# Kernel optimization log

Measured on AMD Instinct MI355X. Metric: run time of the kernel, lower is better.

## Reference

```python
import jax, jax.numpy as jnp
import numpy as np

L, B, T, D, H, F, V = 8, 2, 1024, 1024, 16, 4096, 50257


def _ln(x, w, b):
    m = jnp.mean(x, axis=-1, keepdims=True)
    v = jnp.mean((x - m) ** 2, axis=-1, keepdims=True)
    return (x - m) * jax.lax.rsqrt(v + 1e-5) * w + b


def setup_inputs() -> dict:
    key = jax.random.key(0)
    ks = iter(jax.random.split(key, 16))
    s = jnp.float32(0.02)
    w = lambda shape: jax.random.normal(next(ks), shape, jnp.float32) * s
    return {
        'idx': jax.random.randint(next(ks), (B, T), 0, V, jnp.int32),
        'emb': w((V, D)),
        'pos_emb': w((T, D)),
        'ln1_w': jnp.ones((L, D), jnp.float32),
        'ln1_b': jnp.zeros((L, D), jnp.float32),
        'qkv_w': w((L, D, 3 * D)),
        'qkv_b': jnp.zeros((L, 3 * D), jnp.float32),
        'ln2_w': jnp.ones((L, D), jnp.float32),
        'ln2_b': jnp.zeros((L, D), jnp.float32),
        'fc1_w': w((L, D, F)),
        'fc1_b': jnp.zeros((L, F), jnp.float32),
        'fc2_w': w((L, F, D)),
        'fc2_b': jnp.zeros((L, D), jnp.float32),
        'lnf_w': jnp.ones((D,), jnp.float32),
        'lnf_b': jnp.zeros((D,), jnp.float32),
        'head_w': w((D, V)),
        'head_b': jnp.zeros((V,), jnp.float32),
    }


def reference(idx, emb, pos_emb, ln1_w, ln1_b, qkv_w, qkv_b, ln2_w, ln2_b,
              fc1_w, fc1_b, fc2_w, fc2_b, lnf_w, lnf_b, head_w, head_b):
    b, t = idx.shape
    d = emb.shape[1]
    hd = d // H
    x = emb[idx] + pos_emb[:t]                      # [b,t,d]
    mask = jnp.tril(jnp.ones((t, t), bool))         # causal mask
    inv_scale = jnp.float32(1.0 / (d ** 0.5))       # NOTE: source scales by sqrt(full dim), not head_dim

    def layer(x, p):
        l1w, l1b, qw, qb, l2w, l2b, f1w, f1b, f2w, f2b = p
        h = _ln(x, l1w, l1b)
        qkv = h @ qw + qb                           # [b,t,3d]
        q, k, v = jnp.split(qkv, 3, axis=-1)
        q = q.reshape(b, t, H, hd)
        k = k.reshape(b, t, H, hd)
        v = v.reshape(b, t, H, hd)
        logits = jnp.einsum('bqhe,bkhe->bhqk', q, k) * inv_scale
        logits = jnp.where(mask, logits, -jnp.inf)
        attn = jax.nn.softmax(logits, axis=-1)
        o = jnp.einsum('bhqk,bkhe->bqhe', attn, v).reshape(b, t, d)
        x = x + o                                   # no output projection in source
        h = _ln(x, l2w, l2b)
        h = jax.nn.gelu(h @ f1w + f1b, approximate=False)
        h = jax.nn.gelu(h @ f2w + f2b, approximate=False)  # GELU after fc2 too, per source
        return x + h, None

    x, _ = jax.lax.scan(
        layer, x,
        (ln1_w, ln1_b, qkv_w, qkv_b, ln2_w, ln2_b, fc1_w, fc1_b, fc2_w, fc2_b))
    x = _ln(x, lnf_w, lnf_b)
    return x @ head_w + head_b                      # [b,t,V] logits
```

## Files before the change

kernel.cpp:

```cpp
#include <hip/hip_runtime.h>
#include <math.h>

#define Ln 8
#define Bn 2
#define Tn 1024
#define Dm 1024
#define Hn 16
#define Fm 4096
#define Vn 50257
#define NTOK 2048

typedef unsigned short u16;
typedef u16   u16x8  __attribute__((ext_vector_type(8)));
typedef __bf16 bf16x8 __attribute__((ext_vector_type(8)));
typedef float f32x4  __attribute__((ext_vector_type(4)));

__device__ __forceinline__ u16 f2bf(float f){
  unsigned u = __builtin_bit_cast(unsigned, f);
  u += 0x7FFFu + ((u >> 16) & 1u);
  return (u16)(u >> 16);
}
__device__ __forceinline__ float bf2f(u16 s){
  return __builtin_bit_cast(float, ((unsigned)s) << 16);
}
__device__ __forceinline__ float gelu_f(float v){
  return 0.5f * v * (1.0f + erff(v * 0.70710678118654752440f));
}
__device__ __forceinline__ void gload16(const void* g, void* l){
  __builtin_amdgcn_global_load_lds(
      (const __attribute__((address_space(1))) void*)g,
      (__attribute__((address_space(3))) void*)l, 16, 0, 0);
}

__global__ __launch_bounds__(256) void embed_kernel(const int* __restrict__ idx,
                                                    const float* __restrict__ emb,
                                                    const float* __restrict__ pos,
                                                    float* __restrict__ x){
  int row = blockIdx.x;
  int t = row & (Tn - 1);
  int id = idx[row];
  const float4* e = (const float4*)(emb + (size_t)id * Dm);
  const float4* p = (const float4*)(pos + (size_t)t * Dm);
  float4* o = (float4*)(x + (size_t)row * Dm);
  int i = threadIdx.x;
  float4 a = e[i], b = p[i];
  o[i] = make_float4(a.x + b.x, a.y + b.y, a.z + b.z, a.w + b.w);
}

__global__ __launch_bounds__(256) void ln_kernel(const float* __restrict__ xin,
                                                 const float* __restrict__ w,
                                                 const float* __restrict__ bb,
                                                 u16* __restrict__ out){
  int row = blockIdx.x;
  int t = threadIdx.x;
  float4 v = ((const float4*)(xin + (size_t)row * Dm))[t];
  float s  = v.x + v.y + v.z + v.w;
  float s2 = v.x*v.x + v.y*v.y + v.z*v.z + v.w*v.w;
  #pragma unroll
  for (int off = 1; off < 64; off <<= 1){
    s  += __shfl_xor(s, off);
    s2 += __shfl_xor(s2, off);
  }
  __shared__ float red[8];
  int wv = t >> 6, lane = t & 63;
  if (lane == 0){ red[wv] = s; red[4 + wv] = s2; }
  __syncthreads();
  s  = red[0] + red[1] + red[2] + red[3];
  s2 = red[4] + red[5] + red[6] + red[7];
  float mean = s * (1.0f / Dm);
  float var  = s2 * (1.0f / Dm) - mean * mean;
  float rs = rsqrtf(var + 1e-5f);
  float4 wv4 = ((const float4*)w)[t];
  float4 bv4 = ((const float4*)bb)[t];
  u16 o4[4];
  o4[0] = f2bf((v.x - mean) * rs * wv4.x + bv4.x);
  o4[1] = f2bf((v.y - mean) * rs * wv4.y + bv4.y);
  o4[2] = f2bf((v.z - mean) * rs * wv4.z + bv4.z);
  o4[3] = f2bf((v.w - mean) * rs * wv4.w + bv4.w);
  *(uint2*)(out + (size_t)row * Dm + t * 4) = *(uint2*)o4;
}

__global__ __launch_bounds__(256) void transpose_w(const float* __restrict__ Bw,
                                                   u16* __restrict__ Bt,
                                                   int N, int K, int c0){
  int n0 = blockIdx.x * 64, k0 = blockIdx.y * 64;
  __shared__ float tile[64][66];
  int t = threadIdx.x;
  int rr = t >> 4, nc = (t & 15) * 4;
  #pragma unroll
  for (int u = 0; u < 4; u++){
    int kk = rr + u * 16;
    int gn = c0 + n0 + nc;
    const float* src = Bw + (size_t)(k0 + kk) * N;
    float4 v;
    if (gn + 3 < N) v = *(const float4*)(src + gn);
    else {
      v.x = (gn     < N) ? src[gn]     : 0.0f;
      v.y = (gn + 1 < N) ? src[gn + 1] : 0.0f;
      v.z = (gn + 2 < N) ? src[gn + 2] : 0.0f;
      v.w = (gn + 3 < N) ? src[gn + 3] : 0.0f;
    }
    tile[kk][nc]     = v.x;
    tile[kk][nc + 1] = v.y;
    tile[kk][nc + 2] = v.z;
    tile[kk][nc + 3] = v.w;
  }
  __syncthreads();
  int np = t >> 2, c = t & 3;
  u16* dst = Bt + (size_t)(n0 + np) * K + k0;
  u16 pk[8];
  #pragma unroll
  for (int j = 0; j < 8; j++) pk[j] = f2bf(tile[c*8 + j][np]);
  *(int4*)(dst + c*8) = *(int4*)pk;
  #pragma unroll
  for (int j = 0; j < 8; j++) pk[j] = f2bf(tile[32 + c*8 + j][np]);
  *(int4*)(dst + 32 + c*8) = *(int4*)pk;
}

#define BM 128
#define BN 128
template<int MODE>
__global__ __launch_bounds__(256) void gemm_kernel(const u16* __restrict__ A,
                                                   const u16* __restrict__ Bt,
                                                   const float* __restrict__ bias,
                                                   void* __restrict__ outp,
                                                   float* __restrict__ resid,
                                                   u16* __restrict__ vT,
                                                   int K, int Nout, int c0){
  __shared__ u16 sA[128][64];
  __shared__ u16 sB[128][64];
  int t = threadIdx.x;
  int lane = t & 63, w = t >> 6;
  int wm = w >> 1, wn = w & 1;
  int lr = lane & 15, lg = lane >> 4;
  int m0 = blockIdx.y * BM, n0 = blockIdx.x * BN;

  f32x4 acc[4][4] = {};

  int srow = lane >> 3, scol = (lane & 7) * 8;
  int cswz = ((lr >> 2) & 3) << 4;

  for (int k0 = 0; k0 < K; k0 += 64){
    __syncthreads();
    #pragma unroll
    for (int i = 0; i < 4; i++){
      int rbase = i*32 + w*8;
      int r = rbase + srow;
      int gc = scol ^ (((r >> 2) & 3) << 4);
      gload16(A  + (size_t)(m0 + r) * K + k0 + gc, (char*)&sA[rbase][0]);
      gload16(Bt + (size_t)(n0 + r) * K + k0 + gc, (char*)&sB[rbase][0]);
    }
    __syncthreads();
    #pragma unroll
    for (int kk = 0; kk < 2; kk++){
      bf16x8 af[4], bfr[4];
      #pragma unroll
      for (int i = 0; i < 4; i++) af[i]  = *(const bf16x8*)&sA[wm*64 + i*16 + lr][(kk*32 + lg*8) ^ cswz];
      #pragma unroll
      for (int j = 0; j < 4; j++) bfr[j] = *(const bf16x8*)&sB[wn*64 + j*16 + lr][(kk*32 + lg*8) ^ cswz];
      #pragma unroll
      for (int i = 0; i < 4; i++)
        #pragma unroll
        for (int j = 0; j < 4; j++)
          acc[i][j] = __builtin_amdgcn_mfma_f32_16x16x32_bf16(af[i], bfr[j], acc[i][j], 0, 0, 0);
    }
  }

  #pragma unroll
  for (int i = 0; i < 4; i++){
    int gr0 = m0 + wm*64 + i*16 + lg*4;
    #pragma unroll
    for (int j = 0; j < 4; j++){
      int gc = c0 + n0 + wn*64 + j*16 + lr;
      if (MODE == 3 && gc >= Nout) continue;
      float bb = bias[gc];
      if (MODE == 0 && gc >= 2048){
        int hh = (gc - 2048) >> 6, dd = (gc - 2048) & 63;
        int b_ = gr0 >> 10, tt = gr0 & 1023;
        u16 pk[4];
        #pragma unroll
        for (int r = 0; r < 4; r++) pk[r] = f2bf(acc[i][j][r] + bb);
        *(uint2*)&vT[((size_t)((b_*Hn + hh)*64 + dd))*Tn + tt] = *(uint2*)pk;
        continue;
      }
      #pragma unroll
      for (int r = 0; r < 4; r++){
        float v = acc[i][j][r] + bb;
        size_t oi = (size_t)(gr0 + r) * Nout + gc;
        if (MODE == 0)      ((u16*)outp)[oi] = f2bf(v);
        else if (MODE == 1) ((u16*)outp)[oi] = f2bf(gelu_f(v));
        else if (MODE == 2) resid[oi] = resid[oi] + gelu_f(v);
        else                ((float*)outp)[oi] = v;
      }
    }
  }
}

__global__ __launch_bounds__(256) void attn_mfma(const u16* __restrict__ qkv,
                                                 const u16* __restrict__ vT,
                                                 float* __restrict__ x){
  int bh = blockIdx.x;
  int b = bh >> 4, h_ = bh & 15;
  int qt = blockIdx.y;
  int t = threadIdx.x;
  int w = t >> 6, lane = t & 63;
  int lr = lane & 15, lg = lane >> 4;

  __shared__ u16 sK [2][64][72];
  __shared__ u16 sVt[2][64][72];
  __shared__ u16 sP [64][72];

  const u16* qbase = qkv + ((size_t)(b*Tn + qt*64 + w*16 + lr)) * 3*Dm + h_*64 + lg*8;
  bf16x8 qf[2];
  qf[0] = *(const bf16x8*)(qbase);
  qf[1] = *(const bf16x8*)(qbase + 32);

  f32x4 o_[4] = {};
  float m_[4], l_[4];
  #pragma unroll
  for (int r = 0; r < 4; r++){ m_[r] = -INFINITY; l_[r] = 0.0f; }

  int sr = t >> 2, sc = (t & 3) * 16;
  const u16* kbase = qkv + ((size_t)(b*Tn + sr)) * 3*Dm + Dm + h_*64 + sc;
  const u16* vbase = vT + ((size_t)(bh*64 + sr)) * Tn + sc;
  int4 kr0, kr1, vr0, vr1;

  kr0 = *(const int4*)(kbase);     kr1 = *(const int4*)(kbase + 8);
  vr0 = *(const int4*)(vbase);     vr1 = *(const int4*)(vbase + 8);
  *(int4*)&sK [0][sr][sc]     = kr0;  *(int4*)&sK [0][sr][sc + 8] = kr1;
  *(int4*)&sVt[0][sr][sc]     = vr0;  *(int4*)&sVt[0][sr][sc + 8] = vr1;

  const float sc_ = 0.03125f;
  for (int kt = 0; kt <= qt; kt++){
    int cur = kt & 1;
    if (kt < qt){
      const u16* kb = kbase + (size_t)(kt + 1) * 64 * 3 * Dm;
      const u16* vb = vbase + (kt + 1) * 64;
      kr0 = *(const int4*)(kb);    kr1 = *(const int4*)(kb + 8);
      vr0 = *(const int4*)(vb);    vr1 = *(const int4*)(vb + 8);
    }
    __syncthreads();

    f32x4 s[4] = {};
    #pragma unroll
    for (int kf = 0; kf < 2; kf++){
      #pragma unroll
      for (int nf = 0; nf < 4; nf++){
        bf16x8 kfrag = *(const bf16x8*)&sK[cur][nf*16 + lr][kf*32 + lg*8];
        s[nf] = __builtin_amdgcn_mfma_f32_16x16x32_bf16(qf[kf], kfrag, s[nf], 0, 0, 0);
      }
    }

    bool lastt = (kt == qt);
    float tmax[4] = {-INFINITY, -INFINITY, -INFINITY, -INFINITY};
    #pragma unroll
    for (int nf = 0; nf < 4; nf++)
      #pragma unroll
      for (int r = 0; r < 4; r++){
        float v = s[nf][r] * sc_;
        if (lastt){
          int kkg = nf*16 + lr, qg = w*16 + lg*4 + r;
          if (kkg > qg) v = -INFINITY;
        }
        s[nf][r] = v;
        tmax[r] = fmaxf(tmax[r], v);
      }
    #pragma unroll
    for (int r = 0; r < 4; r++){
      tmax[r] = fmaxf(tmax[r], __shfl_xor(tmax[r], 1));
      tmax[r] = fmaxf(tmax[r], __shfl_xor(tmax[r], 2));
      tmax[r] = fmaxf(tmax[r], __shfl_xor(tmax[r], 4));
      tmax[r] = fmaxf(tmax[r], __shfl_xor(tmax[r], 8));
    }
    float resc[4], psum[4];
    #pragma unroll
    for (int r = 0; r < 4; r++){
      float nm = fmaxf(m_[r], tmax[r]);
      resc[r] = __expf(m_[r] - nm);
      m_[r] = nm;
      psum[r] = 0.0f;
    }
    #pragma unroll
    for (int nf = 0; nf < 4; nf++)
      #pragma unroll
      for (int r = 0; r < 4; r++){
        float pv = __expf(s[nf][r] - m_[r]);
        s[nf][r] = pv;
        psum[r] += pv;
      }
    #pragma unroll
    for (int r = 0; r < 4; r++){
      psum[r] += __shfl_xor(psum[r], 1);
      psum[r] += __shfl_xor(psum[r], 2);
      psum[r] += __shfl_xor(psum[r], 4);
      psum[r] += __shfl_xor(psum[r], 8);
      l_[r] = l_[r] * resc[r] + psum[r];
    }
    #pragma unroll
    for (int df = 0; df < 4; df++)
      #pragma unroll
      for (int r = 0; r < 4; r++)
        o_[df][r] *= resc[r];

    #pragma unroll
    for (int nf = 0; nf < 4; nf++)
      #pragma unroll
      for (int r = 0; r < 4; r++)
        sP[w*16 + lg*4 + r][nf*16 + lr] = f2bf(s[nf][r]);

    #pragma unroll
    for (int kf = 0; kf < 2; kf++){
      bf16x8 pfrag = *(const bf16x8*)&sP[w*16 + lr][kf*32 + lg*8];
      #pragma unroll
      for (int df = 0; df < 4; df++){
        bf16x8 vfrag = *(const bf16x8*)&sVt[cur][df*16 + lr][kf*32 + lg*8];
        o_[df] = __builtin_amdgcn_mfma_f32_16x16x32_bf16(pfrag, vfrag, o_[df], 0, 0, 0);
      }
    }

    if (kt < qt){
      int nxt = cur ^ 1;
      *(int4*)&sK [nxt][sr][sc]     = kr0;  *(int4*)&sK [nxt][sr][sc + 8] = kr1;
      *(int4*)&sVt[nxt][sr][sc]     = vr0;  *(int4*)&sVt[nxt][sr][sc + 8] = vr1;
    }
  }

  float inv[4];
  #pragma unroll
  for (int r = 0; r < 4; r++) inv[r] = 1.0f / l_[r];
  #pragma unroll
  for (int df = 0; df < 4; df++)
    #pragma unroll
    for (int r = 0; r < 4; r++){
      float* xr = x + ((size_t)(b*Tn + qt*64 + w*16 + lg*4 + r)) * Dm + h_*64 + df*16 + lr;
      *xr += o_[df][r] * inv[r];
    }
}

extern "C" void kernel_launch(void* const* d_in, const int* in_sizes, int n_in,
                              void* d_out, int out_size, void* d_ws, size_t ws_size,
                              hipStream_t stream){
  const int*   idx   = (const int*)  d_in[0];
  const float* emb   = (const float*)d_in[1];
  const float* pos   = (const float*)d_in[2];
  const float* ln1w  = (const float*)d_in[3];
  const float* ln1b  = (const float*)d_in[4];
  const float* qkvw  = (const float*)d_in[5];
  const float* qkvb  = (const float*)d_in[6];
  const float* ln2w  = (const float*)d_in[7];
  const float* ln2b  = (const float*)d_in[8];
  const float* fc1w  = (const float*)d_in[9];
  const float* fc1b  = (const float*)d_in[10];
  const float* fc2w  = (const float*)d_in[11];
  const float* fc2b  = (const float*)d_in[12];
  const float* lnfw  = (const float*)d_in[13];
  const float* lnfb  = (const float*)d_in[14];
  const float* headw = (const float*)d_in[15];
  const float* headb = (const float*)d_in[16];
  float* out = (float*)d_out;

  char* ws = (char*)d_ws;
  float* x   = (float*)(ws);
  u16*   h   = (u16*)  (ws + (8u  << 20));
  u16*   qkv = (u16*)  (ws + (12u << 20));
  u16*   f1  = (u16*)  (ws + (24u << 20));
  u16*   Bt  = (u16*)  (ws + (40u << 20));
  u16*   vT  = (u16*)  (ws + (48u << 20));

  embed_kernel<<<NTOK, 256, 0, stream>>>(idx, emb, pos, x);

  for (int l = 0; l < Ln; l++){
    ln_kernel<<<NTOK, 256, 0, stream>>>(x, ln1w + l*Dm, ln1b + l*Dm, h);
    transpose_w<<<dim3(3072/64, Dm/64), 256, 0, stream>>>(qkvw + (size_t)l*Dm*3072, Bt, 3072, Dm, 0);
    gemm_kernel<0><<<dim3(3072/BN, NTOK/BM), 256, 0, stream>>>(h, Bt, qkvb + l*3072, qkv, nullptr, vT, Dm, 3072, 0);
    attn_mfma<<<dim3(Bn*Hn, Tn/64), 256, 0, stream>>>(qkv, vT, x);
    ln_kernel<<<NTOK, 256, 0, stream>>>(x, ln2w + l*Dm, ln2b + l*Dm, h);
    transpose_w<<<dim3(Fm/64, Dm/64), 256, 0, stream>>>(fc1w + (size_t)l*Dm*Fm, Bt, Fm, Dm, 0);
    gemm_kernel<1><<<dim3(Fm/BN, NTOK/BM), 256, 0, stream>>>(h, Bt, fc1b + l*Fm, f1, nullptr, nullptr, Dm, Fm, 0);
    transpose_w<<<dim3(Dm/64, Fm/64), 256, 0, stream>>>(fc2w + (size_t)l*Fm*Dm, Bt, Dm, Fm, 0);
    gemm_kernel<2><<<dim3(Dm/BN, NTOK/BM), 256, 0, stream>>>(f1, Bt, fc2b + l*Dm, nullptr, x, nullptr, Fm, Dm, 0);
  }

  ln_kernel<<<NTOK, 256, 0, stream>>>(x, lnfw, lnfb, h);

  const int CHUNK = 4096;
  for (int c0 = 0; c0 < Vn; c0 += CHUNK){
    int W = Vn - c0; if (W > CHUNK) W = CHUNK;
    int ngx = (W + BN - 1) / BN;
    transpose_w<<<dim3(ngx * 2, Dm/64), 256, 0, stream>>>(headw, Bt, Vn, Dm, c0);
    gemm_kernel<3><<<dim3(ngx, NTOK/BM), 256, 0, stream>>>(h, Bt, headb, out, nullptr, nullptr, Dm, Vn, c0);
  }
}
```

Before: 2.144 ms.

## Reorder attention blocks heaviest-first, prescale Q, raise MFMA priority, single head GEMM

The attention grid is flattened to 512 blocks and ordered so the longest causal query tiles are scheduled first, which targets load imbalance at the tail. The softmax scale is folded into Q when it is loaded, s_setprio brackets the MFMA sections, and the LM-head weight transpose and GEMM run as one launch over the full vocabulary when the workspace is large enough, replacing 13 chunked launch pairs. Folding the scale into Q before rounding to bf16 changes rounding slightly, and the single head path depends on the workspace size check.

```diff
diff --git a/kernel.cpp b/kernel.cpp
--- a/kernel.cpp
+++ b/kernel.cpp
@@ -199,9 +199,11 @@
 __global__ __launch_bounds__(256) void attn_mfma(const u16* __restrict__ qkv,
                                                  const u16* __restrict__ vT,
                                                  float* __restrict__ x){
-  int bh = blockIdx.x;
+  int bid = blockIdx.x;
+  int bh = bid & 31;
+  int j = bid >> 5;
+  int qt = (j < 8) ? (15 - j) : (j - 8);
   int b = bh >> 4, h_ = bh & 15;
-  int qt = blockIdx.y;
   int t = threadIdx.x;
   int w = t >> 6, lane = t & 63;
   int lr = lane & 15, lg = lane >> 4;
@@ -212,25 +214,28 @@
 
   const u16* qbase = qkv + ((size_t)(b*Tn + qt*64 + w*16 + lr)) * 3*Dm + h_*64 + lg*8;
   bf16x8 qf[2];
-  qf[0] = *(const bf16x8*)(qbase);
-  qf[1] = *(const bf16x8*)(qbase + 32);
+  #pragma unroll
+  for (int i = 0; i < 2; i++){
+    u16x8 raw = *(const u16x8*)(qbase + i * 32);
+    #pragma unroll
+    for (int u = 0; u < 8; u++) qf[i][u] = (__bf16)(bf2f(raw[u]) * 0.03125f);
+  }
 
   f32x4 o_[4] = {};
   float m_[4], l_[4];
   #pragma unroll
   for (int r = 0; r < 4; r++){ m_[r] = -INFINITY; l_[r] = 0.0f; }
 
-  int sr = t >> 2, sc = (t & 3) * 16;
-  const u16* kbase = qkv + ((size_t)(b*Tn + sr)) * 3*Dm + Dm + h_*64 + sc;
-  const u16* vbase = vT + ((size_t)(bh*64 + sr)) * Tn + sc;
+  int sr = t >> 2, scc = (t & 3) * 16;
+  const u16* kbase = qkv + ((size_t)(b*Tn + sr)) * 3*Dm + Dm + h_*64 + scc;
+  const u16* vbase = vT + ((size_t)(bh*64 + sr)) * Tn + scc;
   int4 kr0, kr1, vr0, vr1;
 
   kr0 = *(const int4*)(kbase);     kr1 = *(const int4*)(kbase + 8);
   vr0 = *(const int4*)(vbase);     vr1 = *(const int4*)(vbase + 8);
-  *(int4*)&sK [0][sr][sc]     = kr0;  *(int4*)&sK [0][sr][sc + 8] = kr1;
-  *(int4*)&sVt[0][sr][sc]     = vr0;  *(int4*)&sVt[0][sr][sc + 8] = vr1;
-
-  const float sc_ = 0.03125f;
+  *(int4*)&sK [0][sr][scc]     = kr0;  *(int4*)&sK [0][sr][scc + 8] = kr1;
+  *(int4*)&sVt[0][sr][scc]     = vr0;  *(int4*)&sVt[0][sr][scc + 8] = vr1;
+
   for (int kt = 0; kt <= qt; kt++){
     int cur = kt & 1;
     if (kt < qt){
@@ -242,6 +247,7 @@
     __syncthreads();
 
     f32x4 s[4] = {};
+    __builtin_amdgcn_s_setprio(1);
     #pragma unroll
     for (int kf = 0; kf < 2; kf++){
       #pragma unroll
@@ -250,6 +256,7 @@
         s[nf] = __builtin_amdgcn_mfma_f32_16x16x32_bf16(qf[kf], kfrag, s[nf], 0, 0, 0);
       }
     }
+    __builtin_amdgcn_s_setprio(0);
 
     bool lastt = (kt == qt);
     float tmax[4] = {-INFINITY, -INFINITY, -INFINITY, -INFINITY};
@@ -257,7 +264,7 @@
     for (int nf = 0; nf < 4; nf++)
       #pragma unroll
       for (int r = 0; r < 4; r++){
-        float v = s[nf][r] * sc_;
+        float v = s[nf][r];
         if (lastt){
           int kkg = nf*16 + lr, qg = w*16 + lg*4 + r;
           if (kkg > qg) v = -INFINITY;
@@ -308,6 +315,7 @@
       for (int r = 0; r < 4; r++)
         sP[w*16 + lg*4 + r][nf*16 + lr] = f2bf(s[nf][r]);
 
+    __builtin_amdgcn_s_setprio(1);
     #pragma unroll
     for (int kf = 0; kf < 2; kf++){
       bf16x8 pfrag = *(const bf16x8*)&sP[w*16 + lr][kf*32 + lg*8];
@@ -317,11 +325,12 @@
         o_[df] = __builtin_amdgcn_mfma_f32_16x16x32_bf16(pfrag, vfrag, o_[df], 0, 0, 0);
       }
     }
+    __builtin_amdgcn_s_setprio(0);
 
     if (kt < qt){
       int nxt = cur ^ 1;
-      *(int4*)&sK [nxt][sr][sc]     = kr0;  *(int4*)&sK [nxt][sr][sc + 8] = kr1;
-      *(int4*)&sVt[nxt][sr][sc]     = vr0;  *(int4*)&sVt[nxt][sr][sc + 8] = vr1;
+      *(int4*)&sK [nxt][sr][scc]     = kr0;  *(int4*)&sK [nxt][sr][scc + 8] = kr1;
+      *(int4*)&sVt[nxt][sr][scc]     = vr0;  *(int4*)&sVt[nxt][sr][scc + 8] = vr1;
     }
   }
 
@@ -366,6 +375,7 @@
   u16*   f1  = (u16*)  (ws + (24u << 20));
   u16*   Bt  = (u16*)  (ws + (40u << 20));
   u16*   vT  = (u16*)  (ws + (48u << 20));
+  u16*   BtF = (u16*)  (ws + (12u << 20));
 
   embed_kernel<<<NTOK, 256, 0, stream>>>(idx, emb, pos, x);
 
@@ -373,7 +383,7 @@
     ln_kernel<<<NTOK, 256, 0, stream>>>(x, ln1w + l*Dm, ln1b + l*Dm, h);
     transpose_w<<<dim3(3072/64, Dm/64), 256, 0, stream>>>(qkvw + (size_t)l*Dm*3072, Bt, 3072, Dm, 0);
     gemm_kernel<0><<<dim3(3072/BN, NTOK/BM), 256, 0, stream>>>(h, Bt, qkvb + l*3072, qkv, nullptr, vT, Dm, 3072, 0);
-    attn_mfma<<<dim3(Bn*Hn, Tn/64), 256, 0, stream>>>(qkv, vT, x);
+    attn_mfma<<<512, 256, 0, stream>>>(qkv, vT, x);
     ln_kernel<<<NTOK, 256, 0, stream>>>(x, ln2w + l*Dm, ln2b + l*Dm, h);
     transpose_w<<<dim3(Fm/64, Dm/64), 256, 0, stream>>>(fc1w + (size_t)l*Dm*Fm, Bt, Fm, Dm, 0);
     gemm_kernel<1><<<dim3(Fm/BN, NTOK/BM), 256, 0, stream>>>(h, Bt, fc1b + l*Fm, f1, nullptr, nullptr, Dm, Fm, 0);
@@ -383,11 +393,16 @@
 
   ln_kernel<<<NTOK, 256, 0, stream>>>(x, lnfw, lnfb, h);
 
-  const int CHUNK = 4096;
-  for (int c0 = 0; c0 < Vn; c0 += CHUNK){
-    int W = Vn - c0; if (W > CHUNK) W = CHUNK;
-    int ngx = (W + BN - 1) / BN;
-    transpose_w<<<dim3(ngx * 2, Dm/64), 256, 0, stream>>>(headw, Bt, Vn, Dm, c0);
-    gemm_kernel<3><<<dim3(ngx, NTOK/BM), 256, 0, stream>>>(h, Bt, headb, out, nullptr, nullptr, Dm, Vn, c0);
-  }
-}
+  if (ws_size >= (116u << 20)){
+    transpose_w<<<dim3(786, Dm/64), 256, 0, stream>>>(headw, BtF, Vn, Dm, 0);
+    gemm_kernel<3><<<dim3(393, NTOK/BM), 256, 0, stream>>>(h, BtF, headb, out, nullptr, nullptr, Dm, Vn, 0);
+  } else {
+    const int CHUNK = 4096;
+    for (int c0 = 0; c0 < Vn; c0 += CHUNK){
+      int W = Vn - c0; if (W > CHUNK) W = CHUNK;
+      int ngx = (W + BN - 1) / BN;
+      transpose_w<<<dim3(ngx * 2, Dm/64), 256, 0, stream>>>(headw, Bt, Vn, Dm, c0);
+      gemm_kernel<3><<<dim3(ngx, NTOK/BM), 256, 0, stream>>>(h, Bt, headb, out, nullptr, nullptr, Dm, Vn, c0);
+    }
+  }
+}
```

Result: faster. 2.000 ms (-6.7%).
